# Optimization experiments

Measured on AMD Instinct MI355X. Metric: run time of the kernel, lower is better.

The kernel has to match this reference:

```python
import jax, jax.numpy as jnp
import numpy as np

MODES = 256
WIDTH = 64
T_HIST = 1
T_FUT = 1
BATCH = 64
S = 8192


def setup_inputs() -> dict:
    key = jax.random.key(0)
    ks = jax.random.split(key, 12)
    scale = 1.0 / (WIDTH * WIDTH)
    inp = {
        "u": jax.random.normal(ks[0], (BATCH, S, T_HIST), dtype=jnp.float32),
        # lifting layer: Linear(T_HIST+1 -> WIDTH), stored [in, out]
        "fc0_w": jax.random.normal(ks[1], (T_HIST + 1, WIDTH), dtype=jnp.float32) * 0.5,
        "fc0_b": jax.random.normal(ks[2], (WIDTH,), dtype=jnp.float32) * 0.1,
        # 4 spectral conv layers, complex weights stored as real/imag parts
        "sw_r": scale * jax.random.uniform(ks[3], (4, WIDTH, WIDTH, MODES), dtype=jnp.float32),
        "sw_i": scale * jax.random.uniform(ks[4], (4, WIDTH, WIDTH, MODES), dtype=jnp.float32),
        # 4 pointwise (1x1 conv) layers: weight [out,in], bias [out]
        "pw_w": jax.random.normal(ks[5], (4, WIDTH, WIDTH), dtype=jnp.float32) * (1.0 / np.sqrt(WIDTH)),
        "pw_b": jax.random.normal(ks[6], (4, WIDTH), dtype=jnp.float32) * 0.1,
        # projection head
        "fc1_w": jax.random.normal(ks[7], (WIDTH, 128), dtype=jnp.float32) * (1.0 / np.sqrt(WIDTH)),
        "fc1_b": jax.random.normal(ks[8], (128,), dtype=jnp.float32) * 0.1,
        "fc2_w": jax.random.normal(ks[9], (128, T_FUT), dtype=jnp.float32) * (1.0 / np.sqrt(128)),
        "fc2_b": jax.random.normal(ks[10], (T_FUT,), dtype=jnp.float32) * 0.1,
    }
    return inp


def _spectral_conv(x, wr, wi):
    # x: [b, c_in, s] real; weights: [c_in, c_out, MODES] (real/imag parts)
    s = x.shape[-1]
    xf = jnp.fft.rfft(x)                     # [b, c_in, s//2+1] complex
    w = wr + 1j * wi
    om = jnp.einsum('bix,iox->box', xf[:, :, :MODES], w)  # [b, c_out, MODES]
    out_ft = jnp.zeros((x.shape[0], wr.shape[1], s // 2 + 1), dtype=om.dtype)
    out_ft = out_ft.at[:, :, :MODES].set(om)
    return jnp.fft.irfft(out_ft, n=s)        # [b, c_out, s] real


def reference(u, fc0_w, fc0_b, sw_r, sw_i, pw_w, pw_b, fc1_w, fc1_b, fc2_w, fc2_b):
    b, s, _ = u.shape
    grid = jnp.broadcast_to(jnp.linspace(0.0, 1.0, s, dtype=u.dtype)[None, :, None], (b, s, 1))
    x = jnp.concatenate([u, grid], axis=-1)              # [b, s, 2]
    x = x @ fc0_w + fc0_b                                # [b, s, W]
    x = jnp.transpose(x, (0, 2, 1))                      # [b, W, s]
    for l in range(4):
        x1 = _spectral_conv(x, sw_r[l], sw_i[l])
        x2 = jnp.einsum('oi,bis->bos', pw_w[l], x) + pw_b[l][None, :, None]
        x = x1 + x2
        if l < 3:
            x = jax.nn.gelu(x, approximate=False)
    x = jnp.transpose(x, (0, 2, 1))                      # [b, s, W]
    x = jax.nn.gelu(x @ fc1_w + fc1_b, approximate=False)
    x = x @ fc2_w + fc2_b                                # [b, s, T_FUT]
    return x
```

## Files before the change

### kernel.cpp

```cpp
#include <hip/hip_runtime.h>
#include <hip/hip_bf16.h>
#include <math.h>

#define BB 64
#define CC 64
#define SS 8192
#define HS 4096
#define NMODE 256
#define KK2 512

typedef __attribute__((ext_vector_type(8))) short short8;
typedef __attribute__((ext_vector_type(16))) float f32x16;

__device__ __forceinline__ float gelu_exact(float v) {
    return 0.5f * v * (1.0f + erff(v * 0.7071067811865476f));
}
__device__ __forceinline__ float b2f(ushort u) {
    return __uint_as_float(((unsigned int)u) << 16);
}
__device__ __forceinline__ ushort f2b(float v) {
    __hip_bfloat16 h = __float2bfloat16(v);
    return *(ushort*)&h;
}
__device__ __forceinline__ void split2(float v, ushort& h, ushort& l) {
    h = f2b(v);
    l = f2b(v - b2f(h));
}
__device__ __forceinline__ int colk(int c) {
    return (c < 256) ? (c & ~1) : (((c - 256) & ~1) | 1);
}

__global__ void build_T1p(ushort* __restrict__ h, ushort* __restrict__ l) {
    int c = blockIdx.x;
    int n = blockIdx.y * 256 + threadIdx.x;
    int k = colk(c), ri = c & 1;
    int m = (n * k) & (SS - 1);
    float th = (float)m * (6.283185307179586476925f / (float)SS);
    float s, co;
    sincosf(th, &s, &co);
    float v = ri ? -s : co;
    ushort hh, ll;
    split2(v, hh, ll);
    h[(size_t)c * HS + n] = hh;
    l[(size_t)c * HS + n] = ll;
}

__global__ void build_T2r(ushort* __restrict__ h, ushort* __restrict__ l) {
    int n = blockIdx.x;
    int c = blockIdx.y * 256 + threadIdx.x;
    int k = colk(c), ri = c & 1;
    int m = (n * k) & (SS - 1);
    float th = (float)m * (6.283185307179586476925f / (float)SS);
    float s, co;
    sincosf(th, &s, &co);
    float v = ri ? -s : co;
    ushort hh, ll;
    split2(v, hh, ll);
    h[(size_t)n * KK2 + c] = hh;
    l[(size_t)n * KK2 + c] = ll;
}

__global__ void zero_xf(float* __restrict__ p) {
    size_t i = ((size_t)blockIdx.x * 256 + threadIdx.x) * 4;
    *(float4*)&p[i] = make_float4(0.f, 0.f, 0.f, 0.f);
}

__global__ void lift_kernel(const float* __restrict__ u, const float* __restrict__ w0,
                            const float* __restrict__ b0, ushort* __restrict__ Eh,
                            ushort* __restrict__ El, ushort* __restrict__ Oh,
                            ushort* __restrict__ Ol) {
    int n = blockIdx.x * 256 + threadIdx.x;
    int c = blockIdx.y;
    int b = blockIdx.z;
    float g1 = (float)n * (1.0f / (float)(SS - 1));
    float g2 = (float)(n + HS) * (1.0f / (float)(SS - 1));
    float v1 = u[b * SS + n] * w0[c] + g1 * w0[CC + c] + b0[c];
    float v2 = u[b * SS + n + HS] * w0[c] + g2 * w0[CC + c] + b0[c];
    float E = v1 + v2, O = v1 - v2;
    ushort hh, ll;
    size_t idx = (size_t)(b * CC + c) * HS + n;
    split2(E, hh, ll);
    Eh[idx] = hh;
    El[idx] = ll;
    split2(O, hh, ll);
    Oh[idx] = hh;
    Ol[idx] = ll;
}

__global__ __launch_bounds__(256, 3) void dft_mfma(
    const ushort* __restrict__ Eh, const ushort* __restrict__ El,
    const ushort* __restrict__ Oh, const ushort* __restrict__ Ol,
    const ushort* __restrict__ t1h, const ushort* __restrict__ t1l,
    float* __restrict__ Xf) {
    __shared__ __align__(16) ushort SM[16384];
    ushort* As_h = SM;
    ushort* As_l = SM + 4096;
    ushort* Bs_h = SM + 8192;
    ushort* Bs_l = SM + 12288;
    const int t = threadIdx.x;
    const int L = blockIdx.x;
    const int gq = L >> 5, j = L & 31;
    const int c0 = (j >> 3) * 128;
    const int m0 = ((gq & 3) * 8 + (j & 7)) * 128;
    const int kz = (gq >> 2) * 1024;
    const ushort* __restrict__ Ahp = (c0 < 256) ? Eh : Oh;
    const ushort* __restrict__ Alp = (c0 < 256) ? El : Ol;
    const int lane = t & 63, w = t >> 6;
    const int wm = (w >> 1) * 64, wn = (w & 1) * 64;
    const int l32 = lane & 31, lh = lane >> 5;
    const int sr = t >> 1, sh = (t & 1) * 16;
    const int g0 = (t & 1) * 2;
    const int d0 = ((g0 + 0) * 128 + sr) * 8;
    const int d1 = ((g0 + 1) * 128 + sr) * 8;

    f32x16 acc[2][2];
#pragma unroll
    for (int i = 0; i < 2; i++)
#pragma unroll
        for (int jj = 0; jj < 2; jj++) acc[i][jj] = (f32x16)0.f;

    const size_t arow = (size_t)(m0 + sr) * HS;
    const size_t brow = (size_t)(c0 + sr) * HS;
    const int kend = kz + 1024;

    short8 a0h, a1h, a0l, a1l, b0h, b1h, b0l, b1l;
    {
        const size_t ga = arow + kz + sh;
        const size_t gb = brow + kz + sh;
        a0h = *(const short8*)&Ahp[ga];
        a1h = *(const short8*)&Ahp[ga + 8];
        a0l = *(const short8*)&Alp[ga];
        a1l = *(const short8*)&Alp[ga + 8];
        b0h = *(const short8*)&t1h[gb];
        b1h = *(const short8*)&t1h[gb + 8];
        b0l = *(const short8*)&t1l[gb];
        b1l = *(const short8*)&t1l[gb + 8];
    }
    for (int kt = kz; kt < kend; kt += 32) {
        __syncthreads();
        *(short8*)&As_h[d0] = a0h;
        *(short8*)&As_h[d1] = a1h;
        *(short8*)&As_l[d0] = a0l;
        *(short8*)&As_l[d1] = a1l;
        *(short8*)&Bs_h[d0] = b0h;
        *(short8*)&Bs_h[d1] = b1h;
        *(short8*)&Bs_l[d0] = b0l;
        *(short8*)&Bs_l[d1] = b1l;
        __syncthreads();
        const int ktn = (kt + 32 < kend) ? kt + 32 : kz;
        const size_t ga = arow + ktn + sh;
        const size_t gb = brow + ktn + sh;
        a0h = *(const short8*)&Ahp[ga];
        a1h = *(const short8*)&Ahp[ga + 8];
        a0l = *(const short8*)&Alp[ga];
        a1l = *(const short8*)&Alp[ga + 8];
        b0h = *(const short8*)&t1h[gb];
        b1h = *(const short8*)&t1h[gb + 8];
        b0l = *(const short8*)&t1l[gb];
        b1l = *(const short8*)&t1l[gb + 8];
#pragma unroll
        for (int s2 = 0; s2 < 2; s2++) {
            const int kg = s2 * 2 + lh;
            short8 ah[2], al[2], bh2[2], bl2[2];
#pragma unroll
            for (int mt = 0; mt < 2; mt++) {
                int off = (kg * 128 + wm + mt * 32 + l32) * 8;
                ah[mt] = *(const short8*)&As_h[off];
                al[mt] = *(const short8*)&As_l[off];
            }
#pragma unroll
            for (int nt = 0; nt < 2; nt++) {
                int off = (kg * 128 + wn + nt * 32 + l32) * 8;
                bh2[nt] = *(const short8*)&Bs_h[off];
                bl2[nt] = *(const short8*)&Bs_l[off];
            }
#pragma unroll
            for (int nt = 0; nt < 2; nt++)
#pragma unroll
                for (int mt = 0; mt < 2; mt++) {
                    acc[mt][nt] = __builtin_amdgcn_mfma_f32_32x32x16_bf16(ah[mt], bh2[nt], acc[mt][nt], 0, 0, 0);
                    acc[mt][nt] = __builtin_amdgcn_mfma_f32_32x32x16_bf16(ah[mt], bl2[nt], acc[mt][nt], 0, 0, 0);
                    acc[mt][nt] = __builtin_amdgcn_mfma_f32_32x32x16_bf16(al[mt], bh2[nt], acc[mt][nt], 0, 0, 0);
                }
        }
    }
#pragma unroll
    for (int mt = 0; mt < 2; mt++)
#pragma unroll
        for (int nt = 0; nt < 2; nt++) {
            int col = c0 + wn + nt * 32 + l32;
#pragma unroll
            for (int reg = 0; reg < 16; reg++) {
                int row = m0 + wm + mt * 32 + (reg & 3) + 8 * (reg >> 2) + 4 * lh;
                atomicAdd(&Xf[(size_t)row * KK2 + col], acc[mt][nt][reg]);
            }
        }
}

__global__ __launch_bounds__(256) void mode_mix(const float* __restrict__ Xf,
                                                const float* __restrict__ swr,
                                                const float* __restrict__ swi,
                                                ushort* __restrict__ omh,
                                                ushort* __restrict__ oml, int l) {
    int k = threadIdx.x;
    int bg = blockIdx.x * 2;
    int og = blockIdx.y * 2;
    const int cp = ((k & 1) << 8) | ((k >> 1) << 1);
    float ar[2][2] = {}, ai[2][2] = {};
#pragma unroll 2
    for (int i = 0; i < CC; i++) {
        float2 x0 = *(const float2*)&Xf[((size_t)(bg + 0) * CC + i) * KK2 + cp];
        float2 x1 = *(const float2*)&Xf[((size_t)(bg + 1) * CC + i) * KK2 + cp];
        size_t wb = ((size_t)(l * CC + i) * CC + og) * NMODE + k;
        float wr0 = swr[wb], wi0 = swi[wb];
        float wr1 = swr[wb + NMODE], wi1 = swi[wb + NMODE];
        ar[0][0] += x0.x * wr0 - x0.y * wi0;
        ai[0][0] += x0.x * wi0 + x0.y * wr0;
        ar[0][1] += x0.x * wr1 - x0.y * wi1;
        ai[0][1] += x0.x * wi1 + x0.y * wr1;
        ar[1][0] += x1.x * wr0 - x1.y * wi0;
        ai[1][0] += x1.x * wi0 + x1.y * wr0;
        ar[1][1] += x1.x * wr1 - x1.y * wi1;
        ai[1][1] += x1.x * wi1 + x1.y * wr1;
    }
    float ck = (k == 0) ? (1.0f / (float)SS) : (2.0f / (float)SS);
#pragma unroll
    for (int b2 = 0; b2 < 2; b2++)
#pragma unroll
        for (int oo = 0; oo < 2; oo++) {
            float re = ar[b2][oo] * ck;
            float im = ai[b2][oo] * ck;
            ushort hr, lr2, hi2, li2;
            split2(re, hr, lr2);
            split2(im, hi2, li2);
            size_t base = ((size_t)(bg + b2) * CC + og + oo) * KK2 + cp;
            *(ushort2*)&omh[base] = make_ushort2(hr, hi2);
            *(ushort2*)&oml[base] = make_ushort2(lr2, li2);
        }
}

__global__ __launch_bounds__(256, 3) void inv_mfma(
    const ushort* __restrict__ omh, const ushort* __restrict__ oml,
    const ushort* __restrict__ t2h, const ushort* __restrict__ t2l,
    const float* __restrict__ pww, const float* __restrict__ pwb,
    ushort* __restrict__ Eh, ushort* __restrict__ El,
    ushort* __restrict__ Oh, ushort* __restrict__ Ol, int l, int gel) {
    __shared__ __align__(16) ushort SM[12288];
    ushort* As_h = SM;
    ushort* As_l = SM + 4096;
    ushort* Bs_h = SM + 8192;
    ushort* Bs_l = SM + 10240;
    const int t = threadIdx.x;
    const int n0 = blockIdx.x * 64;
    const int row0 = blockIdx.y * 128;
    const int lane = t & 63, w = t >> 6;
    const int wm = (w >> 1) * 64, wn = (w & 1) * 32;
    const int l32 = lane & 31, lh = lane >> 5;
    const int sr = t >> 1, sh = (t & 1) * 16;
    const int g0 = (t & 1) * 2;
    const int dA0 = ((g0 + 0) * 128 + sr) * 8;
    const int dA1 = ((g0 + 1) * 128 + sr) * 8;
    const int srB = (t >> 1) & 63;
    const int dB0 = ((g0 + 0) * 64 + srB) * 8;
    const int dB1 = ((g0 + 1) * 64 + srB) * 8;
    const bool doB = t < 128;

    f32x16 aP[2], aQ[2];
#pragma unroll
    for (int i = 0; i < 2; i++) {
        aP[i] = (f32x16)0.f;
        aQ[i] = (f32x16)0.f;
    }

    const size_t arow = (size_t)(row0 + sr) * KK2;
    const size_t brow = (size_t)(n0 + srB) * KK2;

    short8 a0h, a1h, a0l, a1l, b0h, b1h, b0l, b1l;
    {
        const size_t ga = arow + sh;
        a0h = *(const short8*)&omh[ga];
        a1h = *(const short8*)&omh[ga + 8];
        a0l = *(const short8*)&oml[ga];
        a1l = *(const short8*)&oml[ga + 8];
        if (doB) {
            const size_t gb = brow + sh;
            b0h = *(const short8*)&t2h[gb];
            b1h = *(const short8*)&t2h[gb + 8];
            b0l = *(const short8*)&t2l[gb];
            b1l = *(const short8*)&t2l[gb + 8];
        }
    }
#pragma unroll
    for (int half = 0; half < 2; half++) {
        f32x16* acc = half ? aQ : aP;
        for (int hs8 = 0; hs8 < 8; hs8++) {
            const int hs = half * 8 + hs8;
            __syncthreads();
            *(short8*)&As_h[dA0] = a0h;
            *(short8*)&As_h[dA1] = a1h;
            *(short8*)&As_l[dA0] = a0l;
            *(short8*)&As_l[dA1] = a1l;
            if (doB) {
                *(short8*)&Bs_h[dB0] = b0h;
                *(short8*)&Bs_h[dB1] = b1h;
                *(short8*)&Bs_l[dB0] = b0l;
                *(short8*)&Bs_l[dB1] = b1l;
            }
            __syncthreads();
            const int ktn = (hs + 1 < 16) ? (hs + 1) * 32 : 0;
            const size_t ga = arow + ktn + sh;
            a0h = *(const short8*)&omh[ga];
            a1h = *(const short8*)&omh[ga + 8];
            a0l = *(const short8*)&oml[ga];
            a1l = *(const short8*)&oml[ga + 8];
            if (doB) {
                const size_t gb = brow + ktn + sh;
                b0h = *(const short8*)&t2h[gb];
                b1h = *(const short8*)&t2h[gb + 8];
                b0l = *(const short8*)&t2l[gb];
                b1l = *(const short8*)&t2l[gb + 8];
            }
#pragma unroll
            for (int s2 = 0; s2 < 2; s2++) {
                const int kg = s2 * 2 + lh;
                short8 ah[2], al[2];
#pragma unroll
                for (int mt = 0; mt < 2; mt++) {
                    int off = (kg * 128 + wm + mt * 32 + l32) * 8;
                    ah[mt] = *(const short8*)&As_h[off];
                    al[mt] = *(const short8*)&As_l[off];
                }
                const int offb = (kg * 64 + wn + l32) * 8;
                short8 bh = *(const short8*)&Bs_h[offb];
                short8 bl = *(const short8*)&Bs_l[offb];
#pragma unroll
                for (int mt = 0; mt < 2; mt++) {
                    acc[mt] = __builtin_amdgcn_mfma_f32_32x32x16_bf16(ah[mt], bh, acc[mt], 0, 0, 0);
                    acc[mt] = __builtin_amdgcn_mfma_f32_32x32x16_bf16(ah[mt], bl, acc[mt], 0, 0, 0);
                    acc[mt] = __builtin_amdgcn_mfma_f32_32x32x16_bf16(al[mt], bh, acc[mt], 0, 0, 0);
                }
            }
        }
    }
#pragma unroll
    for (int mt = 0; mt < 2; mt++) {
        f32x16 p = aP[mt];
        aP[mt] = p + aQ[mt];
        aQ[mt] = p - aQ[mt];
    }
    const int bsw = w >> 1;
    const int xbs = t >> 7, xi = (t >> 1) & 63, xseg = (t & 1) * 32;
    const size_t xg = (size_t)(row0 + xbs * 64 + xi) * HS + n0 + xseg;
    const ushort* const srcs[4] = {Eh, El, Oh, Ol};
#pragma unroll
    for (int r = 0; r < 4; r++) {
        const ushort* src = srcs[r];
        const bool isO = (r >= 2), isHi = !(r & 1);
        short8 v0 = *(const short8*)&src[xg];
        short8 v1 = *(const short8*)&src[xg + 8];
        short8 v2 = *(const short8*)&src[xg + 16];
        short8 v3 = *(const short8*)&src[xg + 24];
        __syncthreads();
        {
            ushort* d = &SM[xbs * 4608 + xi * 72 + xseg];
            *(short8*)d = v0;
            *(short8*)(d + 8) = v1;
            *(short8*)(d + 16) = v2;
            *(short8*)(d + 24) = v3;
        }
        __syncthreads();
#pragma unroll
        for (int ks = 0; ks < 4; ks++) {
            short8 pah[2], pal[2], pnh[2], pnl[2];
#pragma unroll
            for (int mt = 0; mt < 2; mt++) {
                int o = mt * 32 + l32;
                const float* pp = &pww[(size_t)(l * CC + o) * CC + ks * 16 + lh * 8];
                float4 pa = *(const float4*)pp;
                float4 pb = *(const float4*)(pp + 4);
                float pv[8] = {pa.x, pa.y, pa.z, pa.w, pb.x, pb.y, pb.z, pb.w};
#pragma unroll
                for (int e = 0; e < 8; e++) {
                    ushort h2, l2;
                    split2(0.5f * pv[e], h2, l2);
                    pah[mt][e] = (short)h2;
                    pal[mt][e] = (short)l2;
                    pnh[mt][e] = (short)(h2 ^ 0x8000);
                    pnl[mt][e] = (short)(l2 ^ 0x8000);
                }
            }
            short8 bf;
            const int rb = bsw * 4608 + (ks * 16 + lh * 8) * 72 + wn + l32;
#pragma unroll
            for (int jj = 0; jj < 8; jj++) bf[jj] = (short)SM[rb + jj * 72];
#pragma unroll
            for (int mt = 0; mt < 2; mt++) {
                aP[mt] = __builtin_amdgcn_mfma_f32_32x32x16_bf16(pah[mt], bf, aP[mt], 0, 0, 0);
                aQ[mt] = __builtin_amdgcn_mfma_f32_32x32x16_bf16(isO ? pnh[mt] : pah[mt], bf, aQ[mt], 0, 0, 0);
                if (isHi) {
                    aP[mt] = __builtin_amdgcn_mfma_f32_32x32x16_bf16(pal[mt], bf, aP[mt], 0, 0, 0);
                    aQ[mt] = __builtin_amdgcn_mfma_f32_32x32x16_bf16(isO ? pnl[mt] : pal[mt], bf, aQ[mt], 0, 0, 0);
                }
            }
        }
    }
#pragma unroll
    for (int mt = 0; mt < 2; mt++)
#pragma unroll
        for (int reg = 0; reg < 16; reg++) {
            int roffs = (reg & 3) + 8 * (reg >> 2) + 4 * lh;
            int o = mt * 32 + roffs;
            float bias = pwb[l * CC + o];
            float uu = aP[mt][reg] + bias;
            float vv = aQ[mt][reg] + bias;
            if (gel) {
                uu = gelu_exact(uu);
                vv = gelu_exact(vv);
            }
            float EE = uu + vv, OO = uu - vv;
            ushort h2, l2;
            size_t gg = (size_t)(row0 + wm + mt * 32 + roffs) * HS + n0 + wn + l32;
            split2(EE, h2, l2);
            Eh[gg] = h2;
            El[gg] = l2;
            split2(OO, h2, l2);
            Oh[gg] = h2;
            Ol[gg] = l2;
        }
}

__global__ __launch_bounds__(256) void head_kernel(
    const ushort* __restrict__ Eh, const ushort* __restrict__ El,
    const ushort* __restrict__ Oh, const ushort* __restrict__ Ol,
    const float* __restrict__ w1, const float* __restrict__ b1,
    const float* __restrict__ w2, const float* __restrict__ b2,
    float* __restrict__ out) {
    __shared__ float Xs[64][64];
    __shared__ float W1s[64][128];
    __shared__ float part[4][64];
    int b = blockIdx.y;
    int n0 = blockIdx.x * 64;
    int tid = threadIdx.x;
    const float sgn = (n0 < HS) ? 1.0f : -1.0f;
    const int nc = n0 & (HS - 1);
    {
        int c = tid >> 2, nq = tid & 3;
        size_t gx = (size_t)(b * CC + c) * HS + nc + nq * 16;
        short8 eh0 = *(const short8*)&Eh[gx], eh1 = *(const short8*)&Eh[gx + 8];
        short8 el0 = *(const short8*)&El[gx], el1 = *(const short8*)&El[gx + 8];
        short8 oh0 = *(const short8*)&Oh[gx], oh1 = *(const short8*)&Oh[gx + 8];
        short8 ol0 = *(const short8*)&Ol[gx], ol1 = *(const short8*)&Ol[gx + 8];
#pragma unroll
        for (int e = 0; e < 8; e++) {
            float e0 = b2f((ushort)eh0[e]) + b2f((ushort)el0[e]);
            float o0 = b2f((ushort)oh0[e]) + b2f((ushort)ol0[e]);
            float e1 = b2f((ushort)eh1[e]) + b2f((ushort)el1[e]);
            float o1 = b2f((ushort)oh1[e]) + b2f((ushort)ol1[e]);
            Xs[c][nq * 16 + e] = 0.5f * (e0 + sgn * o0);
            Xs[c][nq * 16 + 8 + e] = 0.5f * (e1 + sgn * o1);
        }
    }
    float* w1flat = &W1s[0][0];
#pragma unroll
    for (int q = 0; q < 8; q++) {
        int off = q * 1024 + tid * 4;
        *(float4*)&w1flat[off] = *(const float4*)&w1[off];
    }
    __syncthreads();
    int nn = tid & 63, jg = tid >> 6;
    float h[32];
#pragma unroll
    for (int jj = 0; jj < 32; jj++) h[jj] = b1[jg * 32 + jj];
    for (int c = 0; c < 64; c++) {
        float xv = Xs[c][nn];
#pragma unroll
        for (int jj = 0; jj < 32; jj++)
            h[jj] = fmaf(xv, W1s[c][jg * 32 + jj], h[jj]);
    }
    float p = 0.f;
#pragma unroll
    for (int jj = 0; jj < 32; jj++)
        p = fmaf(gelu_exact(h[jj]), w2[jg * 32 + jj], p);
    part[jg][nn] = p;
    __syncthreads();
    if (tid < 64) {
        float v = part[0][tid] + part[1][tid] + part[2][tid] + part[3][tid] + b2[0];
        out[b * SS + n0 + tid] = v;
    }
}

extern "C" void kernel_launch(void* const* d_in, const int* in_sizes, int n_in,
                              void* d_out, int out_size, void* d_ws, size_t ws_size,
                              hipStream_t stream) {
    (void)in_sizes; (void)n_in; (void)out_size; (void)ws_size;
    const float* u = (const float*)d_in[0];
    const float* fc0_w = (const float*)d_in[1];
    const float* fc0_b = (const float*)d_in[2];
    const float* sw_r = (const float*)d_in[3];
    const float* sw_i = (const float*)d_in[4];
    const float* pw_w = (const float*)d_in[5];
    const float* pw_b = (const float*)d_in[6];
    const float* fc1_w = (const float*)d_in[7];
    const float* fc1_b = (const float*)d_in[8];
    const float* fc2_w = (const float*)d_in[9];
    const float* fc2_b = (const float*)d_in[10];
    float* out = (float*)d_out;

    char* ws = (char*)d_ws;
    ushort* Eh = (ushort*)ws;
    ushort* El = (ushort*)(ws + 33554432);
    ushort* Oh = (ushort*)(ws + 67108864);
    ushort* Ol = (ushort*)(ws + 100663296);
    ushort* t1h = (ushort*)(ws + 134217728);
    ushort* t1l = (ushort*)(ws + 138412032);
    ushort* t2h = (ushort*)(ws + 142606336);
    ushort* t2l = (ushort*)(ws + 146800640);
    ushort* omh = (ushort*)(ws + 150994944);
    ushort* oml = (ushort*)(ws + 155189248);
    float* Xf = (float*)(ws + 159383552);

    build_T1p<<<dim3(KK2, HS / 256), 256, 0, stream>>>(t1h, t1l);
    build_T2r<<<dim3(HS, KK2 / 256), 256, 0, stream>>>(t2h, t2l);
    lift_kernel<<<dim3(HS / 256, CC, BB), 256, 0, stream>>>(u, fc0_w, fc0_b, Eh, El,
                                                            Oh, Ol);
    for (int l = 0; l < 4; l++) {
        zero_xf<<<dim3(2048), 256, 0, stream>>>(Xf);
        dft_mfma<<<dim3(512), 256, 0, stream>>>(Eh, El, Oh, Ol, t1h, t1l, Xf);
        mode_mix<<<dim3(BB / 2, CC / 2), 256, 0, stream>>>(Xf, sw_r, sw_i, omh, oml, l);
        inv_mfma<<<dim3(HS / 64, 32), 256, 0, stream>>>(
            omh, oml, t2h, t2l, pw_w, pw_b, Eh, El, Oh, Ol, l, (l < 3) ? 1 : 0);
    }
    head_kernel<<<dim3(SS / 64, BB), 256, 0, stream>>>(Eh, El, Oh, Ol, fc1_w, fc1_b,
                                                       fc2_w, fc2_b, out);
}
```

Measured before the change: 1.399 ms.

## Widen inverse-DFT tile to 128 columns and stage operands via global_load_lds

The inv_mfma kernel now computes a 128x128 output tile per block instead of 128x64, so each wave holds a 2x2 set of MFMA accumulators and the A operand is reused across twice as many columns. Shared-memory staging now uses direct global-to-LDS loads in place of register prefetch followed by LDS stores. The pointwise-weight bf16 split is hoisted out of the per-source loop, and the sign flip for the odd half is applied to the B fragment instead. The cost is higher register and LDS use, so occupancy drops from 3 to 2 blocks per CU and there are half as many blocks; the old register-level prefetch overlap is also gone.

```diff
diff --git a/kernel.cpp b/kernel.cpp
--- a/kernel.cpp
+++ b/kernel.cpp
@@ -28,6 +28,10 @@
 }
 __device__ __forceinline__ int colk(int c) {
     return (c < 256) ? (c & ~1) : (((c - 256) & ~1) | 1);
+}
+__device__ __forceinline__ void dma16(const ushort* g, ushort* l) {
+    __builtin_amdgcn_global_load_lds((const __attribute__((address_space(1))) void*)g,
+                                     (__attribute__((address_space(3))) void*)l, 16, 0, 0);
 }
 
 __global__ void build_T1p(ushort* __restrict__ h, ushort* __restrict__ l) {
@@ -239,194 +243,172 @@
         }
 }
 
-__global__ __launch_bounds__(256, 3) void inv_mfma(
+__global__ __launch_bounds__(256, 2) void inv_mfma(
     const ushort* __restrict__ omh, const ushort* __restrict__ oml,
     const ushort* __restrict__ t2h, const ushort* __restrict__ t2l,
     const float* __restrict__ pww, const float* __restrict__ pwb,
     ushort* __restrict__ Eh, ushort* __restrict__ El,
     ushort* __restrict__ Oh, ushort* __restrict__ Ol, int l, int gel) {
-    __shared__ __align__(16) ushort SM[12288];
+    __shared__ __align__(16) ushort SM[16384];
     ushort* As_h = SM;
     ushort* As_l = SM + 4096;
     ushort* Bs_h = SM + 8192;
-    ushort* Bs_l = SM + 10240;
+    ushort* Bs_l = SM + 12288;
     const int t = threadIdx.x;
-    const int n0 = blockIdx.x * 64;
+    const int n0 = blockIdx.x * 128;
     const int row0 = blockIdx.y * 128;
     const int lane = t & 63, w = t >> 6;
-    const int wm = (w >> 1) * 64, wn = (w & 1) * 32;
+    const int wm = (w >> 1) * 64, wn = (w & 1) * 64;
     const int l32 = lane & 31, lh = lane >> 5;
-    const int sr = t >> 1, sh = (t & 1) * 16;
-    const int g0 = (t & 1) * 2;
-    const int dA0 = ((g0 + 0) * 128 + sr) * 8;
-    const int dA1 = ((g0 + 1) * 128 + sr) * 8;
-    const int srB = (t >> 1) & 63;
-    const int dB0 = ((g0 + 0) * 64 + srB) * 8;
-    const int dB1 = ((g0 + 1) * 64 + srB) * 8;
-    const bool doB = t < 128;
-
-    f32x16 aP[2], aQ[2];
-#pragma unroll
-    for (int i = 0; i < 2; i++) {
-        aP[i] = (f32x16)0.f;
-        aQ[i] = (f32x16)0.f;
-    }
-
-    const size_t arow = (size_t)(row0 + sr) * KK2;
-    const size_t brow = (size_t)(n0 + srB) * KK2;
-
-    short8 a0h, a1h, a0l, a1l, b0h, b1h, b0l, b1l;
-    {
-        const size_t ga = arow + sh;
-        a0h = *(const short8*)&omh[ga];
-        a1h = *(const short8*)&omh[ga + 8];
-        a0l = *(const short8*)&oml[ga];
-        a1l = *(const short8*)&oml[ga + 8];
-        if (doB) {
-            const size_t gb = brow + sh;
-            b0h = *(const short8*)&t2h[gb];
-            b1h = *(const short8*)&t2h[gb + 8];
-            b0l = *(const short8*)&t2l[gb];
-            b1l = *(const short8*)&t2l[gb + 8];
-        }
-    }
+
+    f32x16 aP[2][2], aQ[2][2];
+#pragma unroll
+    for (int i = 0; i < 2; i++)
+#pragma unroll
+        for (int jj = 0; jj < 2; jj++) {
+            aP[i][jj] = (f32x16)0.f;
+            aQ[i][jj] = (f32x16)0.f;
+        }
+
+    const size_t aoff = (size_t)(row0 + lane) * KK2 + w * 8;
+    const size_t boff = (size_t)(n0 + lane) * KK2 + w * 8;
+    const size_t rstep = (size_t)64 * KK2;
+    ushort* dAh = As_h + w * 1024;
+    ushort* dAl = As_l + w * 1024;
+    ushort* dBh = Bs_h + w * 1024;
+    ushort* dBl = Bs_l + w * 1024;
+
 #pragma unroll
     for (int half = 0; half < 2; half++) {
-        f32x16* acc = half ? aQ : aP;
         for (int hs8 = 0; hs8 < 8; hs8++) {
-            const int hs = half * 8 + hs8;
+            const int kt = half * 256 + hs8 * 32;
+            dma16(omh + aoff + kt, dAh);
+            dma16(omh + aoff + rstep + kt, dAh + 512);
+            dma16(oml + aoff + kt, dAl);
+            dma16(oml + aoff + rstep + kt, dAl + 512);
+            dma16(t2h + boff + kt, dBh);
+            dma16(t2h + boff + rstep + kt, dBh + 512);
+            dma16(t2l + boff + kt, dBl);
+            dma16(t2l + boff + rstep + kt, dBl + 512);
             __syncthreads();
-            *(short8*)&As_h[dA0] = a0h;
-            *(short8*)&As_h[dA1] = a1h;
-            *(short8*)&As_l[dA0] = a0l;
-            *(short8*)&As_l[dA1] = a1l;
-            if (doB) {
-                *(short8*)&Bs_h[dB0] = b0h;
-                *(short8*)&Bs_h[dB1] = b1h;
-                *(short8*)&Bs_l[dB0] = b0l;
-                *(short8*)&Bs_l[dB1] = b1l;
-            }
-            __syncthreads();
-            const int ktn = (hs + 1 < 16) ? (hs + 1) * 32 : 0;
-            const size_t ga = arow + ktn + sh;
-            a0h = *(const short8*)&omh[ga];
-            a1h = *(const short8*)&omh[ga + 8];
-            a0l = *(const short8*)&oml[ga];
-            a1l = *(const short8*)&oml[ga + 8];
-            if (doB) {
-                const size_t gb = brow + ktn + sh;
-                b0h = *(const short8*)&t2h[gb];
-                b1h = *(const short8*)&t2h[gb + 8];
-                b0l = *(const short8*)&t2l[gb];
-                b1l = *(const short8*)&t2l[gb + 8];
-            }
 #pragma unroll
             for (int s2 = 0; s2 < 2; s2++) {
                 const int kg = s2 * 2 + lh;
-                short8 ah[2], al[2];
+                short8 ah[2], al[2], bh2[2], bl2[2];
 #pragma unroll
                 for (int mt = 0; mt < 2; mt++) {
                     int off = (kg * 128 + wm + mt * 32 + l32) * 8;
                     ah[mt] = *(const short8*)&As_h[off];
                     al[mt] = *(const short8*)&As_l[off];
                 }
-                const int offb = (kg * 64 + wn + l32) * 8;
-                short8 bh = *(const short8*)&Bs_h[offb];
-                short8 bl = *(const short8*)&Bs_l[offb];
-#pragma unroll
-                for (int mt = 0; mt < 2; mt++) {
-                    acc[mt] = __builtin_amdgcn_mfma_f32_32x32x16_bf16(ah[mt], bh, acc[mt], 0, 0, 0);
-                    acc[mt] = __builtin_amdgcn_mfma_f32_32x32x16_bf16(ah[mt], bl, acc[mt], 0, 0, 0);
-                    acc[mt] = __builtin_amdgcn_mfma_f32_32x32x16_bf16(al[mt], bh, acc[mt], 0, 0, 0);
+#pragma unroll
+                for (int nt = 0; nt < 2; nt++) {
+                    int off = (kg * 128 + wn + nt * 32 + l32) * 8;
+                    bh2[nt] = *(const short8*)&Bs_h[off];
+                    bl2[nt] = *(const short8*)&Bs_l[off];
                 }
-            }
-        }
-    }
-#pragma unroll
-    for (int mt = 0; mt < 2; mt++) {
-        f32x16 p = aP[mt];
-        aP[mt] = p + aQ[mt];
-        aQ[mt] = p - aQ[mt];
-    }
+#pragma unroll
+                for (int nt = 0; nt < 2; nt++)
+#pragma unroll
+                    for (int mt = 0; mt < 2; mt++) {
+                        f32x16* ac = half ? &aQ[mt][nt] : &aP[mt][nt];
+                        *ac = __builtin_amdgcn_mfma_f32_32x32x16_bf16(ah[mt], bh2[nt], *ac, 0, 0, 0);
+                        *ac = __builtin_amdgcn_mfma_f32_32x32x16_bf16(ah[mt], bl2[nt], *ac, 0, 0, 0);
+                        *ac = __builtin_amdgcn_mfma_f32_32x32x16_bf16(al[mt], bh2[nt], *ac, 0, 0, 0);
+                    }
+            }
+            __syncthreads();
+        }
+    }
+#pragma unroll
+    for (int mt = 0; mt < 2; mt++)
+#pragma unroll
+        for (int nt = 0; nt < 2; nt++) {
+            f32x16 p = aP[mt][nt];
+            aP[mt][nt] = p + aQ[mt][nt];
+            aQ[mt][nt] = p - aQ[mt][nt];
+        }
+    short8 pah[4][2], pal[4][2];
+#pragma unroll
+    for (int ks = 0; ks < 4; ks++)
+#pragma unroll
+        for (int mt = 0; mt < 2; mt++) {
+            const float* pp = &pww[(size_t)(l * CC + mt * 32 + l32) * CC + ks * 16 + lh * 8];
+            float4 pa = *(const float4*)pp;
+            float4 pb = *(const float4*)(pp + 4);
+            float pv[8] = {pa.x, pa.y, pa.z, pa.w, pb.x, pb.y, pb.z, pb.w};
+#pragma unroll
+            for (int e = 0; e < 8; e++) {
+                ushort h2, l2;
+                split2(0.5f * pv[e], h2, l2);
+                pah[ks][mt][e] = (short)h2;
+                pal[ks][mt][e] = (short)l2;
+            }
+        }
+    const size_t xsrc = (size_t)(row0 + (w >> 1) * 64 + (w & 1) * 32 + (lane >> 4)) * HS +
+                        n0 + (lane & 15) * 8;
+    ushort* dX = SM + w * 4096;
     const int bsw = w >> 1;
-    const int xbs = t >> 7, xi = (t >> 1) & 63, xseg = (t & 1) * 32;
-    const size_t xg = (size_t)(row0 + xbs * 64 + xi) * HS + n0 + xseg;
     const ushort* const srcs[4] = {Eh, El, Oh, Ol};
 #pragma unroll
     for (int r = 0; r < 4; r++) {
         const ushort* src = srcs[r];
         const bool isO = (r >= 2), isHi = !(r & 1);
-        short8 v0 = *(const short8*)&src[xg];
-        short8 v1 = *(const short8*)&src[xg + 8];
-        short8 v2 = *(const short8*)&src[xg + 16];
-        short8 v3 = *(const short8*)&src[xg + 24];
         __syncthreads();
-        {
-            ushort* d = &SM[xbs * 4608 + xi * 72 + xseg];
-            *(short8*)d = v0;
-            *(short8*)(d + 8) = v1;
-            *(short8*)(d + 16) = v2;
-            *(short8*)(d + 24) = v3;
-        }
+#pragma unroll
+        for (int q = 0; q < 8; q++) dma16(src + xsrc + (size_t)q * 4 * HS, dX + q * 512);
         __syncthreads();
 #pragma unroll
         for (int ks = 0; ks < 4; ks++) {
-            short8 pah[2], pal[2], pnh[2], pnl[2];
-#pragma unroll
-            for (int mt = 0; mt < 2; mt++) {
-                int o = mt * 32 + l32;
-                const float* pp = &pww[(size_t)(l * CC + o) * CC + ks * 16 + lh * 8];
-                float4 pa = *(const float4*)pp;
-                float4 pb = *(const float4*)(pp + 4);
-                float pv[8] = {pa.x, pa.y, pa.z, pa.w, pb.x, pb.y, pb.z, pb.w};
-#pragma unroll
-                for (int e = 0; e < 8; e++) {
-                    ushort h2, l2;
-                    split2(0.5f * pv[e], h2, l2);
-                    pah[mt][e] = (short)h2;
-                    pal[mt][e] = (short)l2;
-                    pnh[mt][e] = (short)(h2 ^ 0x8000);
-                    pnl[mt][e] = (short)(l2 ^ 0x8000);
+            short8 bf[2], nbf[2];
+#pragma unroll
+            for (int nt = 0; nt < 2; nt++) {
+                const int rb = (bsw * 64 + ks * 16 + lh * 8) * 128 + wn + nt * 32 + l32;
+#pragma unroll
+                for (int jj = 0; jj < 8; jj++) bf[nt][jj] = (short)SM[rb + jj * 128];
+                if (isO) {
+#pragma unroll
+                    for (int jj = 0; jj < 8; jj++)
+                        nbf[nt][jj] = (short)(bf[nt][jj] ^ (short)0x8000);
                 }
             }
-            short8 bf;
-            const int rb = bsw * 4608 + (ks * 16 + lh * 8) * 72 + wn + l32;
-#pragma unroll
-            for (int jj = 0; jj < 8; jj++) bf[jj] = (short)SM[rb + jj * 72];
-#pragma unroll
-            for (int mt = 0; mt < 2; mt++) {
-                aP[mt] = __builtin_amdgcn_mfma_f32_32x32x16_bf16(pah[mt], bf, aP[mt], 0, 0, 0);
-                aQ[mt] = __builtin_amdgcn_mfma_f32_32x32x16_bf16(isO ? pnh[mt] : pah[mt], bf, aQ[mt], 0, 0, 0);
-                if (isHi) {
-                    aP[mt] = __builtin_amdgcn_mfma_f32_32x32x16_bf16(pal[mt], bf, aP[mt], 0, 0, 0);
-                    aQ[mt] = __builtin_amdgcn_mfma_f32_32x32x16_bf16(isO ? pnl[mt] : pal[mt], bf, aQ[mt], 0, 0, 0);
+#pragma unroll
+            for (int nt = 0; nt < 2; nt++)
+#pragma unroll
+                for (int mt = 0; mt < 2; mt++) {
+                    aP[mt][nt] = __builtin_amdgcn_mfma_f32_32x32x16_bf16(pah[ks][mt], bf[nt], aP[mt][nt], 0, 0, 0);
+                    aQ[mt][nt] = __builtin_amdgcn_mfma_f32_32x32x16_bf16(pah[ks][mt], isO ? nbf[nt] : bf[nt], aQ[mt][nt], 0, 0, 0);
+                    if (isHi) {
+                        aP[mt][nt] = __builtin_amdgcn_mfma_f32_32x32x16_bf16(pal[ks][mt], bf[nt], aP[mt][nt], 0, 0, 0);
+                        aQ[mt][nt] = __builtin_amdgcn_mfma_f32_32x32x16_bf16(pal[ks][mt], isO ? nbf[nt] : bf[nt], aQ[mt][nt], 0, 0, 0);
+                    }
                 }
-            }
         }
     }
 #pragma unroll
     for (int mt = 0; mt < 2; mt++)
 #pragma unroll
-        for (int reg = 0; reg < 16; reg++) {
-            int roffs = (reg & 3) + 8 * (reg >> 2) + 4 * lh;
-            int o = mt * 32 + roffs;
-            float bias = pwb[l * CC + o];
-            float uu = aP[mt][reg] + bias;
-            float vv = aQ[mt][reg] + bias;
-            if (gel) {
-                uu = gelu_exact(uu);
-                vv = gelu_exact(vv);
-            }
-            float EE = uu + vv, OO = uu - vv;
-            ushort h2, l2;
-            size_t gg = (size_t)(row0 + wm + mt * 32 + roffs) * HS + n0 + wn + l32;
-            split2(EE, h2, l2);
-            Eh[gg] = h2;
-            El[gg] = l2;
-            split2(OO, h2, l2);
-            Oh[gg] = h2;
-            Ol[gg] = l2;
-        }
+        for (int nt = 0; nt < 2; nt++)
+#pragma unroll
+            for (int reg = 0; reg < 16; reg++) {
+                int roffs = (reg & 3) + 8 * (reg >> 2) + 4 * lh;
+                float bias = pwb[l * CC + mt * 32 + roffs];
+                float uu = aP[mt][nt][reg] + bias;
+                float vv = aQ[mt][nt][reg] + bias;
+                if (gel) {
+                    uu = gelu_exact(uu);
+                    vv = gelu_exact(vv);
+                }
+                float EE = uu + vv, OO = uu - vv;
+                ushort h2, l2;
+                size_t gg = (size_t)(row0 + wm + mt * 32 + roffs) * HS + n0 + wn + nt * 32 + l32;
+                split2(EE, h2, l2);
+                Eh[gg] = h2;
+                El[gg] = l2;
+                split2(OO, h2, l2);
+                Oh[gg] = h2;
+                Ol[gg] = l2;
+            }
 }
 
 __global__ __launch_bounds__(256) void head_kernel(
@@ -527,7 +509,7 @@
         zero_xf<<<dim3(2048), 256, 0, stream>>>(Xf);
         dft_mfma<<<dim3(512), 256, 0, stream>>>(Eh, El, Oh, Ol, t1h, t1l, Xf);
         mode_mix<<<dim3(BB / 2, CC / 2), 256, 0, stream>>>(Xf, sw_r, sw_i, omh, oml, l);
-        inv_mfma<<<dim3(HS / 64, 32), 256, 0, stream>>>(
+        inv_mfma<<<dim3(HS / 128, 32), 256, 0, stream>>>(
             omh, oml, t2h, t2l, pw_w, pw_b, Eh, El, Oh, Ol, l, (l < 3) ? 1 : 0);
     }
     head_kernel<<<dim3(SS / 64, BB), 256, 0, stream>>>(Eh, El, Oh, Ol, fc1_w, fc1_b,
```

Result: faster. 1.344 ms (-3.9%).
